# Kernel tuning notes

Hardware: AMD Instinct MI355X
Metric: run time of the kernel (lower is better)

Reference implementation:

```python
import jax, jax.numpy as jnp
import numpy as np

N = 100000
E = 1600000
F_IN = 64
HID = 64
OUT = 64
NEG_SLOPE = 0.2


def _gat_layer(x, src, dst, W_src, W_dst, att_src, att_dst, bias):
    # GATConv (PyG), heads=1, add_self_loops=False
    xs = x @ W_src                      # [N, C] transformed source feats
    xd = x @ W_dst                      # [N, C] transformed dest feats
    a_s = xs @ att_src                  # [N] per-node source logits
    a_d = xd @ att_dst                  # [N] per-node dest logits
    e = a_s[src] + a_d[dst]             # [E]
    e = jnp.where(e > 0, e, NEG_SLOPE * e)  # leaky_relu(0.2)
    # segment softmax over incoming edges of each dst node
    m = jax.ops.segment_max(e, dst, num_segments=N)       # [N]
    ex = jnp.exp(e - m[dst])                                # [E]
    denom = jax.ops.segment_sum(ex, dst, num_segments=N)   # [N]
    alpha = ex / denom[dst]                                 # [E]
    msg = xs[src] * alpha[:, None]                          # [E, C]
    out = jax.ops.segment_sum(msg, dst, num_segments=N)    # [N, C]
    return out + bias


def setup_inputs() -> dict:
    key = jax.random.key(0)
    ks = jax.random.split(key, 16)
    x = jax.random.normal(ks[0], (N, F_IN), dtype=jnp.float32)
    edge_index = jax.random.randint(ks[1], (2, E), 0, N, dtype=jnp.int64)
    s = 1.0 / np.sqrt(F_IN)
    sh = 1.0 / np.sqrt(HID)
    return {
        "x": x,
        "edge_index": edge_index,
        "W_src1": jax.random.normal(ks[2], (F_IN, HID), jnp.float32) * s,
        "W_dst1": jax.random.normal(ks[3], (F_IN, HID), jnp.float32) * s,
        "att_src1": jax.random.normal(ks[4], (HID,), jnp.float32) * sh,
        "att_dst1": jax.random.normal(ks[5], (HID,), jnp.float32) * sh,
        "b_conv1": jnp.zeros((HID,), jnp.float32),
        "W_lin1": jax.random.normal(ks[6], (F_IN, HID), jnp.float32) * s,
        "b_lin1": jnp.zeros((HID,), jnp.float32),
        "W_src2": jax.random.normal(ks[7], (HID, OUT), jnp.float32) * sh,
        "W_dst2": jax.random.normal(ks[8], (HID, OUT), jnp.float32) * sh,
        "att_src2": jax.random.normal(ks[9], (OUT,), jnp.float32) * sh,
        "att_dst2": jax.random.normal(ks[10], (OUT,), jnp.float32) * sh,
        "b_conv2": jnp.zeros((OUT,), jnp.float32),
        "W_lin2": jax.random.normal(ks[11], (HID, OUT), jnp.float32) * sh,
        "b_lin2": jnp.zeros((OUT,), jnp.float32),
    }


def reference(x, edge_index, W_src1, W_dst1, att_src1, att_dst1, b_conv1,
              W_lin1, b_lin1, W_src2, W_dst2, att_src2, att_dst2, b_conv2,
              W_lin2, b_lin2):
    src, dst = edge_index[0], edge_index[1]
    h = _gat_layer(x, src, dst, W_src1, W_dst1, att_src1, att_dst1, b_conv1) \
        + (x @ W_lin1 + b_lin1)
    h = _gat_layer(h, src, dst, W_src2, W_dst2, att_src2, att_dst2, b_conv2) \
        + (h @ W_lin2 + b_lin2)
    # F.normalize(dim=1), eps=1e-12
    norm = jnp.maximum(jnp.linalg.norm(h, axis=1, keepdims=True), 1e-12)
    return h / norm
```

## Files before the change

### kernel.cpp

```cpp
#include <hip/hip_runtime.h>
#include <hip/hip_fp16.h>
#include <math.h>

#define C 64
#define NEG_SLOPE 0.2f
#define LDP 68
#define BN 64
#define CH 8192

__global__ void k_wvec(const float* __restrict__ W, const float* __restrict__ att,
                       float* __restrict__ wv) {
    int k = threadIdx.x;
    float s = 0.f;
    #pragma unroll
    for (int c = 0; c < C; ++c) s = fmaf(W[k * C + c], att[c], s);
    wv[k] = s;
}

__global__ __launch_bounds__(256, 4) void k_transform(
    const float* __restrict__ x,
    const float* __restrict__ Wsrc,
    const float* __restrict__ Wlin,
    const float* __restrict__ att_src,
    const float* __restrict__ wd,
    const float* __restrict__ b_conv,
    const float* __restrict__ b_lin,
    __half* __restrict__ xs_h,
    float* __restrict__ a_s,
    float* __restrict__ a_d,
    float* __restrict__ outbuf,
    int nNodes)
{
    __shared__ float sW[C * C];
    __shared__ float sx[C * LDP];
    __shared__ float swd[C];

    const int tid = threadIdx.x;
    const int tx = tid & 15;
    const int ty = tid >> 4;
    const int tx4 = tx * 4;
    const int n0 = blockIdx.x * 64;

    if (tid < C) swd[tid] = wd[tid];
    #pragma unroll
    for (int j = 0; j < 4; ++j) {
        int idx = tid + j * 256;
        int r = idx >> 4, q = idx & 15;
        *(float4*)&sW[r * C + q * 4] = *(const float4*)&Wsrc[r * C + q * 4];
    }
    #pragma unroll
    for (int j = 0; j < 4; ++j) {
        int idx = tid + j * 256;
        int r = idx >> 4, q = idx & 15;
        int n = n0 + r;
        float4 v = make_float4(0.f, 0.f, 0.f, 0.f);
        if (n < nNodes) v = *(const float4*)&x[(size_t)n * C + q * 4];
        *(float4*)&sx[r * LDP + q * 4] = v;
    }
    __syncthreads();

#define FMA4(XV, W, ACC)            \
    ACC.x = fmaf(XV, W.x, ACC.x);   \
    ACC.y = fmaf(XV, W.y, ACC.y);   \
    ACC.z = fmaf(XV, W.z, ACC.z);   \
    ACC.w = fmaf(XV, W.w, ACC.w);

    float4 accS0 = {0,0,0,0}, accS1 = {0,0,0,0}, accS2 = {0,0,0,0}, accS3 = {0,0,0,0};
    float ad0 = 0.f, ad1 = 0.f, ad2 = 0.f, ad3 = 0.f;

#define KSUB_S(COMP, KOFF)                                          \
    {                                                               \
        float4 ws = *(const float4*)&sW[(k0 + KOFF) * C + tx4];     \
        float wdk = swd[k0 + KOFF];                                 \
        ad0 = fmaf(xr0.COMP, wdk, ad0); FMA4(xr0.COMP, ws, accS0)   \
        ad1 = fmaf(xr1.COMP, wdk, ad1); FMA4(xr1.COMP, ws, accS1)   \
        ad2 = fmaf(xr2.COMP, wdk, ad2); FMA4(xr2.COMP, ws, accS2)   \
        ad3 = fmaf(xr3.COMP, wdk, ad3); FMA4(xr3.COMP, ws, accS3)   \
    }

    #pragma unroll 2
    for (int k0 = 0; k0 < C; k0 += 4) {
        float4 xr0 = *(const float4*)&sx[(ty * 4 + 0) * LDP + k0];
        float4 xr1 = *(const float4*)&sx[(ty * 4 + 1) * LDP + k0];
        float4 xr2 = *(const float4*)&sx[(ty * 4 + 2) * LDP + k0];
        float4 xr3 = *(const float4*)&sx[(ty * 4 + 3) * LDP + k0];
        KSUB_S(x, 0)
        KSUB_S(y, 1)
        KSUB_S(z, 2)
        KSUB_S(w, 3)
    }
#undef KSUB_S

    {
        float4 attv = *(const float4*)&att_src[tx4];
#define EPI_S(R, AS, AD)                                                       \
        {                                                                      \
            int n = n0 + ty * 4 + R;                                           \
            if (n < nNodes) {                                                  \
                union { __half2 h2[2]; uint2 u2; } cv;                         \
                cv.h2[0] = __floats2half2_rn(AS.x, AS.y);                      \
                cv.h2[1] = __floats2half2_rn(AS.z, AS.w);                      \
                *(uint2*)&xs_h[(size_t)n * C + tx4] = cv.u2;                   \
                float p = AS.x * attv.x + AS.y * attv.y                        \
                        + AS.z * attv.z + AS.w * attv.w;                       \
                p += __shfl_xor(p, 8); p += __shfl_xor(p, 4);                  \
                p += __shfl_xor(p, 2); p += __shfl_xor(p, 1);                  \
                if (tx == 0) { a_s[n] = p; a_d[n] = AD; }                      \
            }                                                                  \
        }
        EPI_S(0, accS0, ad0)
        EPI_S(1, accS1, ad1)
        EPI_S(2, accS2, ad2)
        EPI_S(3, accS3, ad3)
#undef EPI_S
    }

    __syncthreads();
    #pragma unroll
    for (int j = 0; j < 4; ++j) {
        int idx = tid + j * 256;
        int r = idx >> 4, q = idx & 15;
        *(float4*)&sW[r * C + q * 4] = *(const float4*)&Wlin[r * C + q * 4];
    }
    __syncthreads();

    float4 accL0 = {0,0,0,0}, accL1 = {0,0,0,0}, accL2 = {0,0,0,0}, accL3 = {0,0,0,0};

#define KSUB_L(COMP, KOFF)                                          \
    {                                                               \
        float4 wl = *(const float4*)&sW[(k0 + KOFF) * C + tx4];     \
        FMA4(xr0.COMP, wl, accL0)                                   \
        FMA4(xr1.COMP, wl, accL1)                                   \
        FMA4(xr2.COMP, wl, accL2)                                   \
        FMA4(xr3.COMP, wl, accL3)                                   \
    }

    #pragma unroll 2
    for (int k0 = 0; k0 < C; k0 += 4) {
        float4 xr0 = *(const float4*)&sx[(ty * 4 + 0) * LDP + k0];
        float4 xr1 = *(const float4*)&sx[(ty * 4 + 1) * LDP + k0];
        float4 xr2 = *(const float4*)&sx[(ty * 4 + 2) * LDP + k0];
        float4 xr3 = *(const float4*)&sx[(ty * 4 + 3) * LDP + k0];
        KSUB_L(x, 0)
        KSUB_L(y, 1)
        KSUB_L(z, 2)
        KSUB_L(w, 3)
    }
#undef KSUB_L
#undef FMA4

    {
        float4 bc = *(const float4*)&b_conv[tx4];
        float4 bl = *(const float4*)&b_lin[tx4];
        float4 bias = make_float4(bc.x + bl.x, bc.y + bl.y, bc.z + bl.z, bc.w + bl.w);
#define EPI_L(R, AL)                                                           \
        {                                                                      \
            int n = n0 + ty * 4 + R;                                           \
            if (n < nNodes) {                                                  \
                float4 vl = make_float4(AL.x + bias.x, AL.y + bias.y,          \
                                        AL.z + bias.z, AL.w + bias.w);         \
                *(float4*)&outbuf[(size_t)n * C + tx4] = vl;                   \
            }                                                                  \
        }
        EPI_L(0, accL0)
        EPI_L(1, accL1)
        EPI_L(2, accL2)
        EPI_L(3, accL3)
#undef EPI_L
    }
}


__global__ __launch_bounds__(256) void k_zero(int* __restrict__ p, int n) {
    for (int i = blockIdx.x * blockDim.x + threadIdx.x; i < n;
         i += gridDim.x * blockDim.x) p[i] = 0;
}

__global__ __launch_bounds__(1024) void k_chist(const int* __restrict__ dst,
                                                int* __restrict__ bcnt,
                                                int* __restrict__ chunkHist,
                                                int nb, int nE) {
    extern __shared__ int lcnt[];
    const int tid = threadIdx.x;
    const int bs = blockDim.x;
    const int e0 = blockIdx.x * CH;
    const int e1 = min(e0 + CH, nE);
    for (int i = tid; i < nb; i += bs) lcnt[i] = 0;
    __syncthreads();
    for (int e = e0 + tid; e < e1; e += bs)
        atomicAdd(&lcnt[dst[e] >> 6], 1);
    __syncthreads();
    int* row = chunkHist + (size_t)blockIdx.x * nb;
    for (int i = tid; i < nb; i += bs) {
        int c = lcnt[i];
        row[i] = c;
        if (c) atomicAdd(&bcnt[i], c);
    }
}

__global__ __launch_bounds__(1024) void k_bscan(const int* __restrict__ cnt,
                                                int* __restrict__ boff,
                                                int* __restrict__ bcur,
                                                int* __restrict__ rowptr,
                                                int nb, int nN, int nE) {
    __shared__ int sd[1024];
    const int t = threadIdx.x;
    int i0 = 2 * t, i1 = 2 * t + 1;
    int c0 = (i0 < nb) ? cnt[i0] : 0;
    int c1 = (i1 < nb) ? cnt[i1] : 0;
    int s = c0 + c1;
    sd[t] = s;
    __syncthreads();
    for (int off = 1; off < 1024; off <<= 1) {
        int v = (t >= off) ? sd[t - off] : 0;
        __syncthreads();
        sd[t] += v;
        __syncthreads();
    }
    int excl = sd[t] - s;
    if (i0 < nb) { boff[i0] = excl;      bcur[i0] = excl; }
    if (i1 < nb) { boff[i1] = excl + c0; bcur[i1] = excl + c0; }
    if (t == 0) { boff[nb] = nE; rowptr[nN] = nE; }
}

__global__ __launch_bounds__(1024) void k_bscatter(const int* __restrict__ src,
                                                   const int* __restrict__ dst,
                                                   const int* __restrict__ chunkHist,
                                                   int* __restrict__ bcur,
                                                   unsigned* __restrict__ packed,
                                                   int nb, int nE) {
    extern __shared__ int lds[];
    int* lcnt  = lds;
    int* lbase = lds + nb;
    const int tid = threadIdx.x;
    const int bs = blockDim.x;
    const int e0 = blockIdx.x * CH;
    const int e1 = min(e0 + CH, nE);

    const int* row = chunkHist + (size_t)blockIdx.x * nb;
    for (int i = tid; i < nb; i += bs) {
        int c = row[i];
        lbase[i] = c ? atomicAdd(&bcur[i], c) : 0;
        lcnt[i] = 0;
    }
    __syncthreads();
    for (int e = e0 + tid; e < e1; e += bs) {
        int d = dst[e];
        int b = d >> 6;
        int pos = lbase[b] + atomicAdd(&lcnt[b], 1);
        packed[pos] = (unsigned)src[e] | ((unsigned)(d & 63) << 17);
    }
}

__global__ __launch_bounds__(256) void k_bsort(
    const unsigned* __restrict__ packed, const int* __restrict__ boff,
    int* __restrict__ rowptr, int* __restrict__ csr_src, int nNodes)
{
    __shared__ int lcnt[BN];
    __shared__ int lcur[BN];
    const int b = blockIdx.x;
    const int base = b * BN;
    const int tid = threadIdx.x;
    const int e0 = boff[b], e1 = boff[b + 1];

    if (tid < BN) lcnt[tid] = 0;
    __syncthreads();
    for (int j = e0 + tid; j < e1; j += 256)
        atomicAdd(&lcnt[packed[j] >> 17], 1);
    __syncthreads();
    if (tid < BN) {
        int v = lcnt[tid];
        int inc = v;
        #pragma unroll
        for (int off = 1; off < BN; off <<= 1) {
            int u = __shfl_up(inc, off, BN);
            if (tid >= off) inc += u;
        }
        int excl = inc - v;
        lcur[tid] = excl;
        int n = base + tid;
        if (n < nNodes) rowptr[n] = e0 + excl;
    }
    __syncthreads();
    for (int j = e0 + tid; j < e1; j += 256) {
        unsigned p = packed[j];
        int pos = atomicAdd(&lcur[p >> 17], 1);
        csr_src[e0 + pos] = (int)(p & 0x1FFFF);
    }
}

template<bool FINAL_NORM>
__global__ __launch_bounds__(256) void k_gat_node(
    const int* __restrict__ rowptr, const int* __restrict__ csr_src,
    const float* __restrict__ a_s, const float* __restrict__ a_d,
    const __half* __restrict__ xs_h, float* __restrict__ outbuf, int nNodes)
{
    __shared__ uint2 sPair[4][64];

    const int tid  = threadIdx.x;
    const int lane = tid & 63;
    const int wslot = tid >> 6;
    const int n = (blockIdx.x * blockDim.x + tid) >> 6;
    if (n >= nNodes) return;
    const int start = rowptr[n], end = rowptr[n + 1];
    if (!FINAL_NORM && start == end) return;
    const float a_dn = a_d[n];

    const int e8 = lane >> 3;
    const int ch = (lane & 7) * 8;

    float acc0 = 0.f, acc1 = 0.f, acc2 = 0.f, acc3 = 0.f;
    float acc4 = 0.f, acc5 = 0.f, acc6 = 0.f, acc7 = 0.f;
    float sloc = 0.f;

    for (int jb = start; jb < end; jb += 64) {
        const int cnt = min(64, end - jb);
        float ex = 0.f; int sidx = 0;
        if (lane < cnt) {
            sidx = csr_src[jb + lane];
            float ev = a_s[sidx] + a_dn;
            ev = ev > 0.f ? ev : NEG_SLOPE * ev;
            ex = __expf(ev);
            sloc += ex;
        }
        sPair[wslot][lane] = make_uint2(__float_as_uint(ex), (unsigned)sidx);

        #pragma unroll 2
        for (int t = 0; t < cnt; t += 8) {
            uint2 pr = sPair[wslot][t + e8];
            float w = __uint_as_float(pr.x);
            int   s = (int)pr.y;
            uint4 raw = *(const uint4*)&xs_h[(size_t)s * C + ch];
            float2 f01 = __half22float2(*(const __half2*)&raw.x);
            float2 f23 = __half22float2(*(const __half2*)&raw.y);
            float2 f45 = __half22float2(*(const __half2*)&raw.z);
            float2 f67 = __half22float2(*(const __half2*)&raw.w);
            acc0 = fmaf(w, f01.x, acc0);
            acc1 = fmaf(w, f01.y, acc1);
            acc2 = fmaf(w, f23.x, acc2);
            acc3 = fmaf(w, f23.y, acc3);
            acc4 = fmaf(w, f45.x, acc4);
            acc5 = fmaf(w, f45.y, acc5);
            acc6 = fmaf(w, f67.x, acc6);
            acc7 = fmaf(w, f67.y, acc7);
        }
    }

#define RED8(M)                                                   \
    acc0 += __shfl_xor(acc0, M); acc1 += __shfl_xor(acc1, M);     \
    acc2 += __shfl_xor(acc2, M); acc3 += __shfl_xor(acc3, M);     \
    acc4 += __shfl_xor(acc4, M); acc5 += __shfl_xor(acc5, M);     \
    acc6 += __shfl_xor(acc6, M); acc7 += __shfl_xor(acc7, M);
    RED8(32) RED8(16) RED8(8)
#undef RED8
    #pragma unroll
    for (int m = 32; m > 0; m >>= 1) sloc += __shfl_xor(sloc, m);

    const float inv = (sloc > 0.f) ? 1.f / sloc : 0.f;

    const int g = lane & 7;
    const int h = (lane >> 3) & 1;
    const int off = g * 8 + h * 4;
    float s0 = h ? acc4 : acc0;
    float s1 = h ? acc5 : acc1;
    float s2 = h ? acc6 : acc2;
    float s3 = h ? acc7 : acc3;

    float4 v = make_float4(0.f, 0.f, 0.f, 0.f);
    if (lane < 16) {
        v = *(const float4*)&outbuf[(size_t)n * C + off];
        v.x = fmaf(s0, inv, v.x);
        v.y = fmaf(s1, inv, v.y);
        v.z = fmaf(s2, inv, v.z);
        v.w = fmaf(s3, inv, v.w);
    }

    if (FINAL_NORM) {
        float vv = (lane < 16) ? (v.x * v.x + v.y * v.y + v.z * v.z + v.w * v.w) : 0.f;
        vv += __shfl_xor(vv, 8);
        vv += __shfl_xor(vv, 4);
        vv += __shfl_xor(vv, 2);
        vv += __shfl_xor(vv, 1);
        float rn = 1.f / fmaxf(sqrtf(vv), 1e-12f);
        v.x *= rn; v.y *= rn; v.z *= rn; v.w *= rn;
    }
    if (lane < 16)
        *(float4*)&outbuf[(size_t)n * C + off] = v;
}

extern "C" void kernel_launch(void* const* d_in, const int* in_sizes, int n_in,
                              void* d_out, int out_size, void* d_ws, size_t ws_size,
                              hipStream_t stream) {
    const float* x  = (const float*)d_in[0];
    const int*   ei = (const int*)d_in[1];
    const int N = in_sizes[0] / C;
    const int E = in_sizes[1] / 2;
    const int* srcIdx = ei;
    const int* dstIdx = ei + E;
    const int NB = (N + BN - 1) / BN;
    const int chunkBlocks = (E + CH - 1) / CH;

    char* w = (char*)d_ws;
    __half*   xs_h   = (__half*)w;   w += (size_t)N * C * 2;
    float*    hbuf   = (float*)w;    w += (size_t)N * C * 4;
    float*    a_s    = (float*)w;    w += (size_t)N * 4;
    float*    a_d    = (float*)w;    w += (size_t)N * 4;
    float*    wvec   = (float*)w;    w += C * 4;
    int*      bcnt   = (int*)w;      w += (size_t)NB * 4;
    int*      boff   = (int*)w;      w += ((size_t)NB + 1) * 4;
    int*      bcur   = (int*)w;      w += (size_t)NB * 4;
    int*      rowptr = (int*)w;      w += ((size_t)N + 1) * 4;
    int*      csr_src= (int*)w;      w += (size_t)E * 4;
    unsigned* packed = (unsigned*)w; w += (size_t)E * 4;
    int*      chist  = (int*)w;      w += (size_t)chunkBlocks * NB * 4;

    const float* Wsrc1 = (const float*)d_in[2];
    const float* Wdst1 = (const float*)d_in[3];
    const float* atts1 = (const float*)d_in[4];
    const float* attd1 = (const float*)d_in[5];
    const float* bcv1  = (const float*)d_in[6];
    const float* Wlin1 = (const float*)d_in[7];
    const float* blin1 = (const float*)d_in[8];
    const float* Wsrc2 = (const float*)d_in[9];
    const float* Wdst2 = (const float*)d_in[10];
    const float* atts2 = (const float*)d_in[11];
    const float* attd2 = (const float*)d_in[12];
    const float* bcv2  = (const float*)d_in[13];
    const float* Wlin2 = (const float*)d_in[14];
    const float* blin2 = (const float*)d_in[15];

    float* out = (float*)d_out;
    const int tblocks = (N + 63) / 64;
    const int nodeWaveBlocks = (N + 3) / 4;

    k_zero<<<8, 256, 0, stream>>>(bcnt, NB);
    k_chist<<<chunkBlocks, 1024, (size_t)NB * 4, stream>>>(dstIdx, bcnt, chist,
                                                           NB, E);
    k_bscan<<<1, 1024, 0, stream>>>(bcnt, boff, bcur, rowptr, NB, N, E);
    k_bscatter<<<chunkBlocks, 1024, (size_t)NB * 8, stream>>>(srcIdx, dstIdx,
                                                              chist, bcur,
                                                              packed, NB, E);
    k_bsort<<<NB, 256, 0, stream>>>(packed, boff, rowptr, csr_src, N);

    k_wvec<<<1, 64, 0, stream>>>(Wdst1, attd1, wvec);
    k_transform<<<tblocks, 256, 0, stream>>>(x, Wsrc1, Wlin1, atts1, wvec,
                                             bcv1, blin1, xs_h, a_s, a_d,
                                             hbuf, N);
    k_gat_node<false><<<nodeWaveBlocks, 256, 0, stream>>>(rowptr, csr_src,
                                                          a_s, a_d, xs_h, hbuf, N);

    k_wvec<<<1, 64, 0, stream>>>(Wdst2, attd2, wvec);
    k_transform<<<tblocks, 256, 0, stream>>>(hbuf, Wsrc2, Wlin2, atts2, wvec,
                                             bcv2, blin2, xs_h, a_s, a_d,
                                             out, N);
    k_gat_node<true><<<nodeWaveBlocks, 256, 0, stream>>>(rowptr, csr_src,
                                                         a_s, a_d, xs_h, out, N);
}
```

Before: 221.6 us.

## Fuse wvec into transform, replace atomic bucket offsets with prefix kernel, pack FMAs

The tiny k_wvec kernel is folded into k_transform, where each block recomputes the Wdst·att_dst vector. The k_zero launch and the global atomics on bcnt and bcur are replaced by a k_cprefix kernel that serially prefix-sums the per-chunk histograms per bucket, so scatter offsets become deterministic. The gather accumulation in k_gat_node uses 2-wide float vectors so the compiler can emit packed FMA and fp16 convert instructions. The changes cut launch count and atomic contention, at the cost of redundant per-block wvec work and a serial loop over chunks in the prefix kernel.

New measurement: 255.0 us. +15.1%, slower.

```diff
diff --git a/kernel.cpp b/kernel.cpp
--- a/kernel.cpp
+++ b/kernel.cpp
@@ -8,21 +8,16 @@
 #define BN 64
 #define CH 8192
 
-__global__ void k_wvec(const float* __restrict__ W, const float* __restrict__ att,
-                       float* __restrict__ wv) {
-    int k = threadIdx.x;
-    float s = 0.f;
-    #pragma unroll
-    for (int c = 0; c < C; ++c) s = fmaf(W[k * C + c], att[c], s);
-    wv[k] = s;
-}
+typedef float  f32x2 __attribute__((ext_vector_type(2)));
+typedef _Float16 f16x2 __attribute__((ext_vector_type(2)));
 
 __global__ __launch_bounds__(256, 4) void k_transform(
     const float* __restrict__ x,
     const float* __restrict__ Wsrc,
     const float* __restrict__ Wlin,
+    const float* __restrict__ Wdst,
+    const float* __restrict__ attd,
     const float* __restrict__ att_src,
-    const float* __restrict__ wd,
     const float* __restrict__ b_conv,
     const float* __restrict__ b_lin,
     __half* __restrict__ xs_h,
@@ -41,7 +36,12 @@
     const int tx4 = tx * 4;
     const int n0 = blockIdx.x * 64;
 
-    if (tid < C) swd[tid] = wd[tid];
+    if (tid < C) {
+        float s = 0.f;
+        #pragma unroll 8
+        for (int c = 0; c < C; ++c) s = fmaf(Wdst[tid * C + c], attd[c], s);
+        swd[tid] = s;
+    }
     #pragma unroll
     for (int j = 0; j < 4; ++j) {
         int idx = tid + j * 256;
@@ -171,13 +171,7 @@
 }
 
 
-__global__ __launch_bounds__(256) void k_zero(int* __restrict__ p, int n) {
-    for (int i = blockIdx.x * blockDim.x + threadIdx.x; i < n;
-         i += gridDim.x * blockDim.x) p[i] = 0;
-}
-
 __global__ __launch_bounds__(1024) void k_chist(const int* __restrict__ dst,
-                                                int* __restrict__ bcnt,
                                                 int* __restrict__ chunkHist,
                                                 int nb, int nE) {
     extern __shared__ int lcnt[];
@@ -191,16 +185,26 @@
         atomicAdd(&lcnt[dst[e] >> 6], 1);
     __syncthreads();
     int* row = chunkHist + (size_t)blockIdx.x * nb;
-    for (int i = tid; i < nb; i += bs) {
-        int c = lcnt[i];
-        row[i] = c;
-        if (c) atomicAdd(&bcnt[i], c);
-    }
+    for (int i = tid; i < nb; i += bs) row[i] = lcnt[i];
+}
+
+__global__ __launch_bounds__(256) void k_cprefix(int* __restrict__ chunkHist,
+                                                 int* __restrict__ bcnt,
+                                                 int nchunks, int nb) {
+    int b = blockIdx.x * blockDim.x + threadIdx.x;
+    if (b >= nb) return;
+    int run = 0;
+    for (int ch = 0; ch < nchunks; ++ch) {
+        int* p = chunkHist + (size_t)ch * nb + b;
+        int v = *p;
+        *p = run;
+        run += v;
+    }
+    bcnt[b] = run;
 }
 
 __global__ __launch_bounds__(1024) void k_bscan(const int* __restrict__ cnt,
                                                 int* __restrict__ boff,
-                                                int* __restrict__ bcur,
                                                 int* __restrict__ rowptr,
                                                 int nb, int nN, int nE) {
     __shared__ int sd[1024];
@@ -218,15 +222,15 @@
         __syncthreads();
     }
     int excl = sd[t] - s;
-    if (i0 < nb) { boff[i0] = excl;      bcur[i0] = excl; }
-    if (i1 < nb) { boff[i1] = excl + c0; bcur[i1] = excl + c0; }
+    if (i0 < nb) boff[i0] = excl;
+    if (i1 < nb) boff[i1] = excl + c0;
     if (t == 0) { boff[nb] = nE; rowptr[nN] = nE; }
 }
 
 __global__ __launch_bounds__(1024) void k_bscatter(const int* __restrict__ src,
                                                    const int* __restrict__ dst,
                                                    const int* __restrict__ chunkHist,
-                                                   int* __restrict__ bcur,
+                                                   const int* __restrict__ boff,
                                                    unsigned* __restrict__ packed,
                                                    int nb, int nE) {
     extern __shared__ int lds[];
@@ -239,8 +243,7 @@
 
     const int* row = chunkHist + (size_t)blockIdx.x * nb;
     for (int i = tid; i < nb; i += bs) {
-        int c = row[i];
-        lbase[i] = c ? atomicAdd(&bcur[i], c) : 0;
+        lbase[i] = boff[i] + row[i];
         lcnt[i] = 0;
     }
     __syncthreads();
@@ -309,8 +312,7 @@
     const int e8 = lane >> 3;
     const int ch = (lane & 7) * 8;
 
-    float acc0 = 0.f, acc1 = 0.f, acc2 = 0.f, acc3 = 0.f;
-    float acc4 = 0.f, acc5 = 0.f, acc6 = 0.f, acc7 = 0.f;
+    f32x2 a01 = {0.f, 0.f}, a23 = {0.f, 0.f}, a45 = {0.f, 0.f}, a67 = {0.f, 0.f};
     float sloc = 0.f;
 
     for (int jb = start; jb < end; jb += 64) {
@@ -331,20 +333,20 @@
             float w = __uint_as_float(pr.x);
             int   s = (int)pr.y;
             uint4 raw = *(const uint4*)&xs_h[(size_t)s * C + ch];
-            float2 f01 = __half22float2(*(const __half2*)&raw.x);
-            float2 f23 = __half22float2(*(const __half2*)&raw.y);
-            float2 f45 = __half22float2(*(const __half2*)&raw.z);
-            float2 f67 = __half22float2(*(const __half2*)&raw.w);
-            acc0 = fmaf(w, f01.x, acc0);
-            acc1 = fmaf(w, f01.y, acc1);
-            acc2 = fmaf(w, f23.x, acc2);
-            acc3 = fmaf(w, f23.y, acc3);
-            acc4 = fmaf(w, f45.x, acc4);
-            acc5 = fmaf(w, f45.y, acc5);
-            acc6 = fmaf(w, f67.x, acc6);
-            acc7 = fmaf(w, f67.y, acc7);
+            f32x2 w2 = {w, w};
+            f32x2 f01 = __builtin_convertvector(__builtin_bit_cast(f16x2, raw.x), f32x2);
+            f32x2 f23 = __builtin_convertvector(__builtin_bit_cast(f16x2, raw.y), f32x2);
+            f32x2 f45 = __builtin_convertvector(__builtin_bit_cast(f16x2, raw.z), f32x2);
+            f32x2 f67 = __builtin_convertvector(__builtin_bit_cast(f16x2, raw.w), f32x2);
+            a01 = __builtin_elementwise_fma(w2, f01, a01);
+            a23 = __builtin_elementwise_fma(w2, f23, a23);
+            a45 = __builtin_elementwise_fma(w2, f45, a45);
+            a67 = __builtin_elementwise_fma(w2, f67, a67);
         }
     }
+
+    float acc0 = a01[0], acc1 = a01[1], acc2 = a23[0], acc3 = a23[1];
+    float acc4 = a45[0], acc5 = a45[1], acc6 = a67[0], acc7 = a67[1];
 
 #define RED8(M)                                                   \
     acc0 += __shfl_xor(acc0, M); acc1 += __shfl_xor(acc1, M);     \
@@ -405,10 +407,8 @@
     float*    hbuf   = (float*)w;    w += (size_t)N * C * 4;
     float*    a_s    = (float*)w;    w += (size_t)N * 4;
     float*    a_d    = (float*)w;    w += (size_t)N * 4;
-    float*    wvec   = (float*)w;    w += C * 4;
     int*      bcnt   = (int*)w;      w += (size_t)NB * 4;
     int*      boff   = (int*)w;      w += ((size_t)NB + 1) * 4;
-    int*      bcur   = (int*)w;      w += (size_t)NB * 4;
     int*      rowptr = (int*)w;      w += ((size_t)N + 1) * 4;
     int*      csr_src= (int*)w;      w += (size_t)E * 4;
     unsigned* packed = (unsigned*)w; w += (size_t)E * 4;
@@ -433,25 +433,22 @@
     const int tblocks = (N + 63) / 64;
     const int nodeWaveBlocks = (N + 3) / 4;
 
-    k_zero<<<8, 256, 0, stream>>>(bcnt, NB);
-    k_chist<<<chunkBlocks, 1024, (size_t)NB * 4, stream>>>(dstIdx, bcnt, chist,
-                                                           NB, E);
-    k_bscan<<<1, 1024, 0, stream>>>(bcnt, boff, bcur, rowptr, NB, N, E);
+    k_chist<<<chunkBlocks, 1024, (size_t)NB * 4, stream>>>(dstIdx, chist, NB, E);
+    k_cprefix<<<(NB + 255) / 256, 256, 0, stream>>>(chist, bcnt, chunkBlocks, NB);
+    k_bscan<<<1, 1024, 0, stream>>>(bcnt, boff, rowptr, NB, N, E);
     k_bscatter<<<chunkBlocks, 1024, (size_t)NB * 8, stream>>>(srcIdx, dstIdx,
-                                                              chist, bcur,
+                                                              chist, boff,
                                                               packed, NB, E);
     k_bsort<<<NB, 256, 0, stream>>>(packed, boff, rowptr, csr_src, N);
 
-    k_wvec<<<1, 64, 0, stream>>>(Wdst1, attd1, wvec);
-    k_transform<<<tblocks, 256, 0, stream>>>(x, Wsrc1, Wlin1, atts1, wvec,
-                                             bcv1, blin1, xs_h, a_s, a_d,
+    k_transform<<<tblocks, 256, 0, stream>>>(x, Wsrc1, Wlin1, Wdst1, attd1,
+                                             atts1, bcv1, blin1, xs_h, a_s, a_d,
                                              hbuf, N);
     k_gat_node<false><<<nodeWaveBlocks, 256, 0, stream>>>(rowptr, csr_src,
                                                           a_s, a_d, xs_h, hbuf, N);
 
-    k_wvec<<<1, 64, 0, stream>>>(Wdst2, attd2, wvec);
-    k_transform<<<tblocks, 256, 0, stream>>>(hbuf, Wsrc2, Wlin2, atts2, wvec,
-                                             bcv2, blin2, xs_h, a_s, a_d,
+    k_transform<<<tblocks, 256, 0, stream>>>(hbuf, Wsrc2, Wlin2, Wdst2, attd2,
+                                             atts2, bcv2, blin2, xs_h, a_s, a_d,
                                              out, N);
     k_gat_node<true><<<nodeWaveBlocks, 256, 0, stream>>>(rowptr, csr_src,
                                                          a_s, a_d, xs_h, out, N);
```
